# Kernel optimization log

Measured on AMD Instinct MI355X. Metric: run time of the kernel, lower is better.

## Reference

```python
import jax, jax.numpy as jnp
import numpy as np

# ---- constants hard-coded in the torch module ----
NEG_EPS = 1e-30          # eps used in log clamps
TAU = 0.35               # near-field temperature (getattr default)
K0 = 128                 # near-field band width
C_EMBD, N_HEADS, RANK = 768, 12, 32
B, T = 1, 2048


def _lin(k, fin, fout):
    lim = 1.0 / np.sqrt(fin)
    return jax.random.uniform(k, (fin, fout), jnp.float32, -lim, lim)


def _bias(k, fin, fout):
    lim = 1.0 / np.sqrt(fin)
    return jax.random.uniform(k, (fout,), jnp.float32, -lim, lim)


def setup_inputs() -> dict:
    key = jax.random.key(0)
    ks = jax.random.split(key, 24)
    C, H, R = C_EMBD, N_HEADS, RANK
    return {
        "x": jax.random.normal(ks[0], (B, T, C), jnp.float32),
        "Wq_w": _lin(ks[1], C, C), "Wq_b": _bias(ks[2], C, C),
        "Wk_w": _lin(ks[3], C, C), "Wk_b": _bias(ks[4], C, C),
        "Wv_w": _lin(ks[5], C, C), "Wv_b": _bias(ks[6], C, C),
        "Wo_w": _lin(ks[7], C, C), "Wo_b": _bias(ks[8], C, C),
        "Pq_w": _lin(ks[9], C, R),
        "Pk_w": _lin(ks[10], C, R),
        "Pv_w": _lin(ks[11], C, R),
        "up_w": _lin(ks[12], R, C),
        "gate_u": jax.random.normal(ks[13], (H, C // H), jnp.float32),
        "gate_b": jnp.zeros((H,), jnp.float32),
        "Wz_w": _lin(ks[14], 4 * C, C), "Wz_b": _bias(ks[15], 4 * C, C),
    }


def reference(x, Wq_w, Wq_b, Wk_w, Wk_b, Wv_w, Wv_b, Wo_w, Wo_b,
              Pq_w, Pk_w, Pv_w, up_w, gate_u, gate_b, Wz_w, Wz_b):
    Bx, Tx, C = x.shape
    H = gate_u.shape[0]
    D = C // H
    R = Pq_w.shape[1]
    k0 = min(K0, Tx - 1)
    kernel = k0 + 1
    b_scalar = -np.log(max(Tx, 1)).astype(np.float32) if hasattr(np.log(1.0), 'astype') else -np.log(max(Tx, 1))
    b_scalar = jnp.float32(-np.log(max(Tx, 1)))

    # 0) projections + heads
    Q = x @ Wq_w + Wq_b
    K = x @ Wk_w + Wk_b
    V = x @ Wv_w + Wv_b
    heads = lambda z: z.reshape(Bx, Tx, H, D).transpose(0, 2, 1, 3)  # (B,H,T,D)
    Qh, Kh, Vh = heads(Q), heads(K), heads(V)

    idx = jnp.arange(Tx)
    causal = idx[None, :] <= idx[:, None]                  # (T,T)
    band = causal & ((idx[:, None] - idx[None, :]) <= k0)  # banded causal

    # 1) low-rank EA + sigmoid + LASER seed
    Qr, Kr, Vr = Q @ Pq_w, K @ Pk_w, V @ Pv_w              # (B,T,R)
    S = (Qr @ Kr.transpose(0, 2, 1)) * (1.0 / np.sqrt(R))  # (B,T,T)
    # masked logits were -1e9 -> sigmoid == 0 exactly in fp32
    A_seed = jnp.where(causal[None], jax.nn.sigmoid(S * S + b_scalar), 0.0)
    # running causal max over keys, per feature (== amax of causally masked keys)
    m_seed = jax.lax.cummax(Vr, axis=1)                    # (B,T,R)
    Yr = jnp.einsum('bij,bjr->bir', A_seed, jnp.exp(Vr)) * jnp.exp(-m_seed)
    H0 = (jnp.log(jnp.maximum(Yr, NEG_EPS)) + m_seed) @ up_w  # (B,T,C)

    # 2a) near-field banded causal attention (cos^2 / tau, sigmoid, LASER)
    l2n = lambda z: z / jnp.maximum(jnp.linalg.norm(z, axis=-1, keepdims=True), 1e-12)
    cos = jnp.einsum('bhid,bhjd->bhij', l2n(Qh), l2n(Kh))  # (B,H,T,T)
    A_near = jnp.where(band[None, None], jax.nn.sigmoid(cos * cos / TAU + b_scalar), 0.0)
    # sliding-window (width kernel, past-only) max of V per feature
    m_near = jax.lax.reduce_window(
        Vh, -jnp.inf, jax.lax.max,
        window_dimensions=(1, 1, kernel, 1), window_strides=(1, 1, 1, 1),
        padding=[(0, 0), (0, 0), (kernel - 1, 0), (0, 0)])   # (B,H,T,D)
    V_exp = jnp.exp(Vh - m_near)
    Y_near = jnp.einsum('bhij,bhjd->bhid', A_near, V_exp)
    H_near = jnp.log(jnp.maximum(Y_near, NEG_EPS)) + m_near

    # 2b) far-field hierarchical levels: source truncates mid-loop; the
    # accumulator H_far_total_h is initialized to zeros -> contributes zero.
    Ht_h = H_near                                          # (B,H,T,D)

    # 3) head-wise sigmoid gating
    g = jax.nn.sigmoid(jnp.einsum('bhtd,hd->bht', Ht_h, gate_u) + gate_b[None, :, None])
    Ht_h = Ht_h * g[..., None]
    Htilde = Ht_h.transpose(0, 2, 1, 3).reshape(Bx, Tx, C)

    # 4) GRU blend (Wz consumes 4*C features)
    z = jax.nn.sigmoid(jnp.concatenate([x, H0, Htilde, H0 * Htilde], axis=-1) @ Wz_w + Wz_b)
    H_out = (1.0 - z) * H0 + z * Htilde
    return H_out @ Wo_w + Wo_b
```

## Files before the change

### kernel.cpp

```cpp
#include <hip/hip_runtime.h>
#include <math.h>

static constexpr float B_SCALAR    = -7.6246189861593985f;
static constexpr float INV_TAU     = 2.8571428571428571f;
static constexpr float INV_SQRT_R  = 0.17677669529663687f;

typedef __attribute__((ext_vector_type(8))) short bf16x8;
typedef __attribute__((ext_vector_type(4))) float f32x4;

__device__ __forceinline__ unsigned short f2b(float f) {
    union { float f; unsigned int u; } v; v.f = f;
    unsigned int r = v.u + 0x7fffu + ((v.u >> 16) & 1u);
    return (unsigned short)(r >> 16);
}
__device__ __forceinline__ float b2f(unsigned short u) {
    union { unsigned int i; float f; } v; v.i = ((unsigned int)u) << 16; return v.f;
}

typedef const __attribute__((address_space(1))) unsigned int* gp1_t;
typedef __attribute__((address_space(3))) unsigned int* lp3_t;
__device__ __forceinline__ void gload16(const unsigned short* g, unsigned short* l) {
    __builtin_amdgcn_global_load_lds((gp1_t)g, (lp3_t)l, 16, 0, 0);
}

__device__ __forceinline__ bf16x8 frag128(const unsigned short* base, int row, int elem) {
    int byte = (row * 128 + elem * 2) ^ ((row & 7) << 4);
    return *(const bf16x8*)((const char*)base + byte);
}
__device__ __forceinline__ bf16x8 frag384(const unsigned short* base, int row, int elem) {
    int byte = (row * 384 + elem * 2) ^ ((row & 7) << 4);
    return *(const bf16x8*)((const char*)base + byte);
}

template<int MODE, int KZ>
__global__ __launch_bounds__(256) void gemm_mfma(
    const unsigned short* __restrict__ A0, const unsigned short* __restrict__ A1,
    const unsigned short* __restrict__ A2,
    const unsigned short* __restrict__ Bt, const float* __restrict__ bias,
    float* __restrict__ outf, unsigned short* __restrict__ outb,
    float* __restrict__ pbuf, int K, int ldo)
{
    __shared__ unsigned short As[2][64*64];
    __shared__ unsigned short Bs[2][128*64];
    const int tid = threadIdx.x;
    const int lane = tid & 63, wid = tid >> 6;
    const int wr = wid >> 1, wc = wid & 1;
    const int fr = lane & 15, fq = lane >> 4;
    const int lin = blockIdx.y * gridDim.x + blockIdx.x;
    const int chunk = (gridDim.x * gridDim.y) >> 3;
    const int sw = (lin & 7) * chunk + (lin >> 3);
    const int n0 = (sw / gridDim.y) * 128, m0 = (sw % gridDim.y) * 64;
    const int kz = blockIdx.z;
    const int kslice = K / KZ;
    const int kbase = kz * kslice;
    const int nt = kslice / 64;

    f32x4 acc[2][4];
#pragma unroll
    for (int mi = 0; mi < 2; ++mi)
#pragma unroll
        for (int ni = 0; ni < 4; ++ni) acc[mi][ni] = (f32x4){0.f, 0.f, 0.f, 0.f};

    auto stage = [&](int buf, int k0) {
        if (MODE == 1 && k0 >= 2304) {
            int k0l = k0 - 2304;
#pragma unroll
            for (int i = 0; i < 2; ++i) {
                int cb = i * 256 + wid * 64, c = cb + lane;
                int r = c >> 3, col = ((c & 7) ^ (r & 7)) * 8;
                bf16x8 a8 = *(const bf16x8*)&A1[(size_t)(m0 + r) * 768 + k0l + col];
                bf16x8 b8 = *(const bf16x8*)&A2[(size_t)(m0 + r) * 768 + k0l + col];
                bf16x8 p8;
#pragma unroll
                for (int e = 0; e < 8; ++e)
                    p8[e] = (short)f2b(b2f((unsigned short)a8[e]) * b2f((unsigned short)b8[e]));
                *(bf16x8*)&As[buf][(size_t)c * 8] = p8;
            }
        } else {
            const unsigned short* Ap;
            int k0l, ldA;
            if (MODE == 1) {
                int p = k0 / 768;
                Ap = (p == 0) ? A0 : (p == 1) ? A1 : A2;
                k0l = k0 - p * 768; ldA = 768;
            } else { Ap = A0; k0l = k0; ldA = K; }
#pragma unroll
            for (int i = 0; i < 2; ++i) {
                int cb = i * 256 + wid * 64, c = cb + lane;
                int r = c >> 3;
                int col = ((c & 7) ^ (r & 7)) * 8;
                gload16(Ap + (size_t)(m0 + r) * ldA + k0l + col, &As[buf][cb * 8]);
            }
        }
#pragma unroll
        for (int i = 0; i < 4; ++i) {
            int cb = i * 256 + wid * 64, c = cb + lane;
            int r = c >> 3;
            int col = ((c & 7) ^ (r & 7)) * 8;
            gload16(Bt + (size_t)(n0 + r) * K + k0 + col, &Bs[buf][cb * 8]);
        }
    };

    stage(0, kbase);
    asm volatile("s_waitcnt vmcnt(0) lgkmcnt(0)" ::: "memory");
    __builtin_amdgcn_s_barrier();
    __builtin_amdgcn_sched_barrier(0);

    int cur = 0;
    for (int t = 0; t < nt; ++t) {
        if (t + 1 < nt) stage(cur ^ 1, kbase + (t + 1) * 64);
#pragma unroll
        for (int kk = 0; kk < 64; kk += 32) {
            bf16x8 af[2], bfr[4];
#pragma unroll
            for (int mi = 0; mi < 2; ++mi)
                af[mi] = frag128(As[cur], wr*32 + mi*16 + fr, kk + fq*8);
#pragma unroll
            for (int ni = 0; ni < 4; ++ni)
                bfr[ni] = frag128(Bs[cur], wc*64 + ni*16 + fr, kk + fq*8);
#pragma unroll
            for (int mi = 0; mi < 2; ++mi)
#pragma unroll
                for (int ni = 0; ni < 4; ++ni)
                    acc[mi][ni] = __builtin_amdgcn_mfma_f32_16x16x32_bf16(
                        af[mi], bfr[ni], acc[mi][ni], 0, 0, 0);
        }
        asm volatile("s_waitcnt vmcnt(0) lgkmcnt(0)" ::: "memory");
        __builtin_amdgcn_s_barrier();
        __builtin_amdgcn_sched_barrier(0);
        cur ^= 1;
    }
#pragma unroll
    for (int mi = 0; mi < 2; ++mi)
#pragma unroll
        for (int ni = 0; ni < 4; ++ni)
#pragma unroll
            for (int v = 0; v < 4; ++v) {
                int m = m0 + wr*32 + mi*16 + fq*4 + v;
                int n = n0 + wc*64 + ni*16 + fr;
                float val = acc[mi][ni][v];
                if (KZ > 1) {
                    pbuf[((size_t)kz * 2048 + m) * 768 + n] = val;
                } else {
                    float vv = val + bias[n];
                    outf[(size_t)m * ldo + n] = vv;
                    if (MODE == 0) outb[(size_t)m * ldo + n] = f2b(vv);
                }
            }
}

__global__ __launch_bounds__(256) void wz_combine(
    const float* __restrict__ pbuf, const float* __restrict__ bz,
    const float* __restrict__ h0, const float* __restrict__ htl,
    unsigned short* __restrict__ outb)
{
    int i = blockIdx.x * 256 + threadIdx.x;
    if (i >= 2048*768/4) return;
    float4 s = *(const float4*)&pbuf[i*4];
    float4 p1 = *(const float4*)&pbuf[1536*1024 + i*4];
    float4 p2 = *(const float4*)&pbuf[2*1536*1024 + i*4];
    float4 p3 = *(const float4*)&pbuf[3*1536*1024 + i*4];
    s.x += p1.x + p2.x + p3.x; s.y += p1.y + p2.y + p3.y;
    s.z += p1.z + p2.z + p3.z; s.w += p1.w + p2.w + p3.w;
    float4 b = *(const float4*)&bz[(i % 192) * 4];
    float4 a = *(const float4*)&h0[i*4];
    float4 t = *(const float4*)&htl[i*4];
    float z0 = 1.f/(1.f+expf(-(s.x+b.x))), z1 = 1.f/(1.f+expf(-(s.y+b.y)));
    float z2 = 1.f/(1.f+expf(-(s.z+b.z))), z3 = 1.f/(1.f+expf(-(s.w+b.w)));
    outb[i*4+0] = f2b((1.f-z0)*a.x + z0*t.x);
    outb[i*4+1] = f2b((1.f-z1)*a.y + z1*t.y);
    outb[i*4+2] = f2b((1.f-z2)*a.z + z2*t.z);
    outb[i*4+3] = f2b((1.f-z3)*a.w + z3*t.w);
}

__global__ __launch_bounds__(256) void prep_all(
    const float* __restrict__ x, unsigned short* __restrict__ xb,
    const float* __restrict__ wq, const float* __restrict__ wk,
    const float* __restrict__ wv, unsigned short* __restrict__ wqkvT,
    const float* __restrict__ wz, unsigned short* __restrict__ wzT,
    const float* __restrict__ wo, unsigned short* __restrict__ woT,
    const float* __restrict__ pq, const float* __restrict__ pk,
    const float* __restrict__ pv, unsigned short* __restrict__ pT,
    const float* __restrict__ bq, const float* __restrict__ bk,
    const float* __restrict__ bv, float* __restrict__ bqkv)
{
    __shared__ float tile[32][33];
    int b = blockIdx.x;
    if (b < 1536) {
        int i = b * 256 + threadIdx.x;
        float4 v = *(const float4*)&x[i * 4];
        xb[i*4+0] = f2b(v.x); xb[i*4+1] = f2b(v.y);
        xb[i*4+2] = f2b(v.z); xb[i*4+3] = f2b(v.w);
        return;
    }
    b -= 1536;
    const float* src; unsigned short* dst; int K, N, tb;
    if (b < 1728) {
        int sel = b / 576;
        src = (sel == 0) ? wq : (sel == 1) ? wk : wv;
        dst = wqkvT + (size_t)sel * 768 * 768;
        K = 768; N = 768; tb = b - sel * 576;
    } else if (b < 4032) {
        src = wz; dst = wzT; K = 3072; N = 768; tb = b - 1728;
    } else if (b < 4608) {
        src = wo; dst = woT; K = 768; N = 768; tb = b - 4032;
    } else if (b < 4680) {
        int sel = (b - 4608) / 24;
        src = (sel == 0) ? pq : (sel == 1) ? pk : pv;
        dst = pT + (size_t)sel * 32 * 768;
        K = 768; N = 32; tb = (b - 4608) % 24;
    } else {
        int n = (b - 4680) * 256 + threadIdx.x;
        if (n < 2304)
            bqkv[n] = (n < 768) ? bq[n] : (n < 1536) ? bk[n - 768] : bv[n - 1536];
        return;
    }
    int kt = K / 32;
    int kb = (tb % kt) * 32, nb = (tb / kt) * 32;
    int tx = threadIdx.x & 31, ty = threadIdx.x >> 5;
#pragma unroll
    for (int s = 0; s < 32; s += 8)
        tile[ty + s][tx] = src[(size_t)(kb + ty + s) * N + nb + tx];
    __syncthreads();
#pragma unroll
    for (int s = 0; s < 32; s += 8)
        dst[(size_t)(nb + ty + s) * K + kb + tx] = f2b(tile[tx][ty + s]);
}

__device__ void lowrank_body(int b, unsigned char* smem,
    const unsigned short* __restrict__ qkvb, const unsigned short* __restrict__ pT,
    float* __restrict__ pbuf)
{
    unsigned short (*As)[128*64] = (unsigned short(*)[128*64])smem;
    unsigned short (*Bs)[32*64]  = (unsigned short(*)[32*64])(smem + 32768);
    const int tid = threadIdx.x, lane = tid & 63, wid = tid >> 6;
    const int fr = lane & 15, fq = lane >> 4;
    const int m0 = (b & 15) * 128;
    const int sel = (b >> 4) % 3, kz = b / 48;
    const int kbase = kz * 192;

    f32x4 acc[2][2];
#pragma unroll
    for (int mi = 0; mi < 2; ++mi)
#pragma unroll
        for (int ni = 0; ni < 2; ++ni) acc[mi][ni] = (f32x4){0.f,0.f,0.f,0.f};

    auto stage = [&](int buf, int k0) {
#pragma unroll
        for (int i = 0; i < 4; ++i) {
            int cb = i * 256 + wid * 64, c = cb + lane;
            int r = c >> 3, col = ((c & 7) ^ (r & 7)) * 8;
            gload16(qkvb + (size_t)(m0 + r) * 2304 + sel*768 + k0 + col, &As[buf][cb * 8]);
        }
        {
            int cb = wid * 64, c = cb + lane;
            int r = c >> 3, col = ((c & 7) ^ (r & 7)) * 8;
            gload16(pT + (size_t)sel * 32*768 + (size_t)r * 768 + k0 + col, &Bs[buf][cb * 8]);
        }
    };

    stage(0, kbase);
    asm volatile("s_waitcnt vmcnt(0)" ::: "memory");
    __builtin_amdgcn_s_barrier();
    __builtin_amdgcn_sched_barrier(0);

    int cur = 0;
    for (int t = 0; t < 3; ++t) {
        if (t + 1 < 3) stage(cur ^ 1, kbase + (t + 1) * 64);
#pragma unroll
        for (int kk = 0; kk < 64; kk += 32) {
            bf16x8 a[2], bb[2];
#pragma unroll
            for (int mi = 0; mi < 2; ++mi)
                a[mi] = frag128(As[cur], wid*32 + mi*16 + fr, kk + fq*8);
#pragma unroll
            for (int ni = 0; ni < 2; ++ni)
                bb[ni] = frag128(Bs[cur], ni*16 + fr, kk + fq*8);
#pragma unroll
            for (int mi = 0; mi < 2; ++mi)
#pragma unroll
                for (int ni = 0; ni < 2; ++ni)
                    acc[mi][ni] = __builtin_amdgcn_mfma_f32_16x16x32_bf16(
                        a[mi], bb[ni], acc[mi][ni], 0, 0, 0);
        }
        asm volatile("s_waitcnt vmcnt(0)" ::: "memory");
        __builtin_amdgcn_s_barrier();
        __builtin_amdgcn_sched_barrier(0);
        cur ^= 1;
    }
#pragma unroll
    for (int mi = 0; mi < 2; ++mi)
#pragma unroll
        for (int ni = 0; ni < 2; ++ni)
#pragma unroll
            for (int v = 0; v < 4; ++v) {
                int m = m0 + wid*32 + mi*16 + fq*4 + v;
                int n = ni*16 + fr;
                pbuf[((size_t)(kz*3 + sel) * 2048 + m) * 32 + n] = acc[mi][ni][v];
            }
}

__device__ void norms_slide_body(int b, unsigned char* smem,
    const float* __restrict__ qkv,
    unsigned short* __restrict__ qhatb, unsigned short* __restrict__ khatb,
    float* __restrict__ mnear, unsigned short* __restrict__ vexptb)
{
    int tid = threadIdx.x;
    if (b < 6144) {
        int w = b * 4 + (tid >> 6);
        int lane = tid & 63;
        int t = w / 12, h = w - t * 12;
        float q = qkv[t*2304 + h*64 + lane];
        float k = qkv[t*2304 + 768 + h*64 + lane];
        float sq = q*q, sk = k*k;
#pragma unroll
        for (int off = 32; off; off >>= 1) { sq += __shfl_xor(sq, off); sk += __shfl_xor(sk, off); }
        float iq = 1.f / fmaxf(sqrtf(sq), 1e-12f);
        float ik = 1.f / fmaxf(sqrtf(sk), 1e-12f);
        qhatb[(size_t)t*768 + h*64 + lane] = f2b(q * iq);
        khatb[(size_t)t*768 + h*64 + lane] = f2b(k * ik);
        return;
    }
    b -= 6144;
    float (*vs)[64] = (float(*)[64])smem;
    int c0 = (b % 12) * 64, t0 = (b / 12) * 64;
#pragma unroll
    for (int s = 0; s < 12; ++s) {
        int idx = tid + s * 256;
        int rr = idx >> 4, c4 = (idx & 15) * 4;
        int t = t0 - 128 + rr;
        float4 v4;
        if (t < 0) v4 = make_float4(-INFINITY, -INFINITY, -INFINITY, -INFINITY);
        else       v4 = *(const float4*)&qkv[t*2304 + 1536 + c0 + c4];
        *(float4*)&vs[rr][c4] = v4;
    }
    __syncthreads();
    int c = tid & 63, tg = tid >> 6;
    const int TG = tg * 16;
    float core = -INFINITY;
    for (int s = TG + 15; s <= TG + 128; ++s) core = fmaxf(core, vs[s][c]);
    float head[16], tail[16];
    head[15] = -INFINITY;
    float hs = -INFINITY;
#pragma unroll
    for (int u = 14; u >= 0; --u) { hs = fmaxf(hs, vs[TG + u][c]); head[u] = hs; }
    tail[0] = -INFINITY;
    float ts = -INFINITY;
#pragma unroll
    for (int u = 1; u <= 15; ++u) { ts = fmaxf(ts, vs[TG + 128 + u][c]); tail[u] = ts; }
#pragma unroll
    for (int u = 0; u < 16; ++u) {
        int tl = TG + u;
        float m = fmaxf(fmaxf(core, head[u]), tail[u]);
        float v = vs[tl + 128][c];
        int t = t0 + tl;
        mnear[(size_t)t*768 + c0 + c] = m;
        vexptb[(size_t)(c0 + c) * 2048 + t] = f2b(expf(v - m));
    }
}

__global__ __launch_bounds__(256) void lrns_pack(
    const unsigned short* __restrict__ qkvb, const unsigned short* __restrict__ pT,
    float* __restrict__ plr, const float* __restrict__ qkv,
    unsigned short* __restrict__ qhatb, unsigned short* __restrict__ khatb,
    float* __restrict__ mnear, unsigned short* __restrict__ vexptb)
{
    __shared__ unsigned char smem[49152];
    int b = blockIdx.x;
    if (b < 192) lowrank_body(b, smem, qkvb, pT, plr);
    else         norms_slide_body(b - 192, smem, qkv, qhatb, khatb, mnear, vexptb);
}

__global__ __launch_bounds__(256) void lowrank_post(
    const float* __restrict__ pbuf,
    unsigned short* __restrict__ qrb, unsigned short* __restrict__ krb,
    unsigned short* __restrict__ evtb, float* __restrict__ ms)
{
    int b = blockIdx.x, tid = threadIdx.x;
    if (b < 512) {
        int idx = b * 256 + tid;
        int sel = idx >> 16, rem = idx & 65535;
        float s = pbuf[(size_t)(0*3 + sel)*65536 + rem]
                + pbuf[(size_t)(1*3 + sel)*65536 + rem]
                + pbuf[(size_t)(2*3 + sel)*65536 + rem]
                + pbuf[(size_t)(3*3 + sel)*65536 + rem];
        if (sel == 0) qrb[rem] = f2b(s * INV_SQRT_R);
        else          krb[rem] = f2b(s);
        return;
    }
    __shared__ float part[256];
    int r = b - 512;
    int t0 = tid * 8;
    float sv[8], v[8];
    float run = -INFINITY;
#pragma unroll
    for (int e = 0; e < 8; ++e) {
        int t = t0 + e;
        float s = pbuf[(size_t)(0*3 + 2)*65536 + t*32 + r]
                + pbuf[(size_t)(1*3 + 2)*65536 + t*32 + r]
                + pbuf[(size_t)(2*3 + 2)*65536 + t*32 + r]
                + pbuf[(size_t)(3*3 + 2)*65536 + t*32 + r];
        sv[e] = s;
        run = fmaxf(run, s);
        v[e] = run;
    }
    part[tid] = run;
    __syncthreads();
    for (int off = 1; off < 256; off <<= 1) {
        float other = (tid >= off) ? part[tid - off] : -INFINITY;
        __syncthreads();
        part[tid] = fmaxf(part[tid], other);
        __syncthreads();
    }
    float excl = (tid > 0) ? part[tid - 1] : -INFINITY;
#pragma unroll
    for (int e = 0; e < 8; ++e) {
        int t = t0 + e;
        ms[t*32 + r] = fmaxf(v[e], excl);
        evtb[(size_t)r * 2048 + t] = f2b(expf(sv[e]));
    }
}

__device__ void seed_body(int it, int jc, unsigned char* smem,
    const unsigned short* __restrict__ qrb, const unsigned short* __restrict__ krb,
    const unsigned short* __restrict__ evtb, float* __restrict__ partial)
{
    const int i0 = it * 128, j0 = jc * 128;
    unsigned short* Qs = (unsigned short*)smem;
    unsigned short* Ks = (unsigned short*)(smem + 8192);
    unsigned short* Es = (unsigned short*)(smem + 16384);
    unsigned short* Ps = (unsigned short*)(smem + 24576);
    const int tid = threadIdx.x, lane = tid & 63, wid = tid >> 6;
    const int fr = lane & 15, fq = lane >> 4;

#pragma unroll
    for (int s = 0; s < 2; ++s) {
        int cb = s * 256 + wid * 64;
        int c = cb + lane;
        int r = c >> 2, col = (c & 3) * 8;
        gload16(qrb + (size_t)(i0 + r) * 32 + col, &Qs[cb * 8]);
        gload16(krb + (size_t)(j0 + r) * 32 + col, &Ks[cb * 8]);
    }
#pragma unroll
    for (int s = 0; s < 2; ++s) {
        int c = s * 256 + tid;
        int rr = c >> 4, cc = c & 15;
        bf16x8 v = *(const bf16x8*)&evtb[(size_t)rr * 2048 + j0 + cc * 8];
        int byte = (rr * 256 + cc * 16) ^ ((rr & 7) << 4);
        *(bf16x8*)((char*)Es + byte) = v;
    }
    __syncthreads();

    const int wr = wid >> 1, wc = wid & 1;
    bf16x8 af[4], bk[4];
#pragma unroll
    for (int mi = 0; mi < 4; ++mi)
        af[mi] = *(const bf16x8*)&Qs[(wr*64 + mi*16 + fr)*32 + fq*8];
#pragma unroll
    for (int ni = 0; ni < 4; ++ni)
        bk[ni] = *(const bf16x8*)&Ks[(wc*64 + ni*16 + fr)*32 + fq*8];
#pragma unroll
    for (int mi = 0; mi < 4; ++mi)
#pragma unroll
        for (int ni = 0; ni < 4; ++ni) {
            f32x4 s4 = __builtin_amdgcn_mfma_f32_16x16x32_bf16(
                af[mi], bk[ni], (f32x4){0.f,0.f,0.f,0.f}, 0, 0, 0);
#pragma unroll
            for (int v = 0; v < 4; ++v) {
                int row = wr*64 + mi*16 + fq*4 + v;
                int col = wc*64 + ni*16 + fr;
                float a = 0.f;
                if (j0 + col <= i0 + row) {
                    float s = s4[v];
                    a = 1.f / (1.f + expf(-(s*s + B_SCALAR)));
                }
                int byte = (row * 256 + col * 2) ^ ((row & 7) << 4);
                *(unsigned short*)((char*)Ps + byte) = f2b(a);
            }
        }
    __syncthreads();

    f32x4 yacc[2][2];
#pragma unroll
    for (int mi = 0; mi < 2; ++mi)
#pragma unroll
        for (int nf = 0; nf < 2; ++nf) yacc[mi][nf] = (f32x4){0.f,0.f,0.f,0.f};
#pragma unroll
    for (int ks = 0; ks < 4; ++ks) {
        bf16x8 pa[2], eb[2];
#pragma unroll
        for (int mi = 0; mi < 2; ++mi) {
            int row = wid*32 + mi*16 + fr;
            int byte = (row * 256 + ks * 64 + fq * 16) ^ ((row & 7) << 4);
            pa[mi] = *(const bf16x8*)((const char*)Ps + byte);
        }
#pragma unroll
        for (int nf = 0; nf < 2; ++nf) {
            int rrow = nf*16 + fr;
            int byte = (rrow * 256 + ks * 64 + fq * 16) ^ ((rrow & 7) << 4);
            eb[nf] = *(const bf16x8*)((const char*)Es + byte);
        }
#pragma unroll
        for (int mi = 0; mi < 2; ++mi)
#pragma unroll
            for (int nf = 0; nf < 2; ++nf)
                yacc[mi][nf] = __builtin_amdgcn_mfma_f32_16x16x32_bf16(
                    pa[mi], eb[nf], yacc[mi][nf], 0, 0, 0);
    }
    float* pout = partial + ((size_t)(it*16 + jc) * 128) * 32;
#pragma unroll
    for (int mi = 0; mi < 2; ++mi)
#pragma unroll
        for (int nf = 0; nf < 2; ++nf)
#pragma unroll
            for (int v = 0; v < 4; ++v) {
                int row = wid*32 + mi*16 + fq*4 + v;
                int col = nf*16 + fr;
                pout[row*32 + col] = yacc[mi][nf][v];
            }
}

__device__ void near_body(int it, int hh, unsigned char* smem,
    const unsigned short* __restrict__ qhatb, const unsigned short* __restrict__ khatb,
    const unsigned short* __restrict__ vexptb, const float* __restrict__ mnear,
    const float* __restrict__ gu, const float* __restrict__ gb,
    float* __restrict__ hn, unsigned short* __restrict__ htlb)
{
    unsigned short* Qs  = (unsigned short*)smem;
    unsigned short* KPs = (unsigned short*)(smem + 8192);
    unsigned short* Vst = (unsigned short*)(smem + 32768);
    const int i0 = it * 64;
    const int tid = threadIdx.x, lane = tid & 63, wid = tid >> 6;
    const int fr = lane & 15, fq = lane >> 4;

#pragma unroll
    for (int i = 0; i < 2; ++i) {
        int cb = i * 256 + wid * 64, c = cb + lane;
        int r = c >> 3, col = ((c & 7) ^ (r & 7)) * 8;
        gload16(qhatb + (size_t)(i0 + r) * 768 + hh*64 + col, &Qs[cb * 8]);
    }
#pragma unroll
    for (int i = 0; i < 6; ++i) {
        int cb = i * 256 + wid * 64, c = cb + lane;
        int r = c >> 3, col = ((c & 7) ^ (r & 7)) * 8;
        int j = i0 - 128 + r; if (j < 0) j = 0;
        gload16(khatb + (size_t)j * 768 + hh*64 + col, &KPs[cb * 8]);
    }
#pragma unroll
    for (int i = 0; i < 6; ++i) {
        int cb = i * 256 + wid * 64, c = cb + lane;
        int d = c / 24, cc = c - d * 24;
        int ccp = (cc & 24) | ((cc & 7) ^ (d & 7));
        int t = i0 - 128 + ccp * 8; if (t < 0) t = 0;
        gload16(vexptb + (size_t)(hh*64 + d) * 2048 + t, &Vst[cb * 8]);
    }
    __syncthreads();

    f32x4 sacc[4][3];
#pragma unroll
    for (int mi = 0; mi < 4; ++mi)
#pragma unroll
        for (int ni = 0; ni < 3; ++ni) sacc[mi][ni] = (f32x4){0.f,0.f,0.f,0.f};
#pragma unroll
    for (int kt = 0; kt < 2; ++kt) {
        int kk = kt * 32;
        bf16x8 qa[4], kb[3];
#pragma unroll
        for (int mi = 0; mi < 4; ++mi)
            qa[mi] = frag128(Qs, mi*16 + fr, kk + fq*8);
#pragma unroll
        for (int ni = 0; ni < 3; ++ni)
            kb[ni] = frag128(KPs, wid*48 + ni*16 + fr, kk + fq*8);
#pragma unroll
        for (int mi = 0; mi < 4; ++mi)
#pragma unroll
            for (int ni = 0; ni < 3; ++ni)
                sacc[mi][ni] = __builtin_amdgcn_mfma_f32_16x16x32_bf16(
                    qa[mi], kb[ni], sacc[mi][ni], 0, 0, 0);
    }
    __syncthreads();

#pragma unroll
    for (int mi = 0; mi < 4; ++mi)
#pragma unroll
        for (int ni = 0; ni < 3; ++ni)
#pragma unroll
            for (int v = 0; v < 4; ++v) {
                int il = mi*16 + fq*4 + v;
                int jl = wid*48 + ni*16 + fr;
                float s = sacc[mi][ni][v];
                float a = 0.f;
                if (jl >= il && jl <= il + 128 && (i0 - 128 + jl) >= 0)
                    a = 1.f / (1.f + expf(-(s*s*INV_TAU + B_SCALAR)));
                int byte = (il * 384 + jl * 2) ^ ((il & 7) << 4);
                *(unsigned short*)((char*)KPs + byte) = f2b(a);
            }
    __syncthreads();

    f32x4 yacc[4];
#pragma unroll
    for (int nf = 0; nf < 4; ++nf) yacc[nf] = (f32x4){0.f,0.f,0.f,0.f};
#pragma unroll
    for (int ks = 0; ks < 6; ++ks) {
        int kk = ks * 32;
        bf16x8 pa = frag384(KPs, wid*16 + fr, kk + fq*8);
        bf16x8 vb[4];
#pragma unroll
        for (int nf = 0; nf < 4; ++nf)
            vb[nf] = frag384(Vst, nf*16 + fr, kk + fq*8);
#pragma unroll
        for (int nf = 0; nf < 4; ++nf)
            yacc[nf] = __builtin_amdgcn_mfma_f32_16x16x32_bf16(pa, vb[nf], yacc[nf], 0, 0, 0);
    }

    float hv[4][4];
    float sp[4] = {0.f, 0.f, 0.f, 0.f};
#pragma unroll
    for (int nf = 0; nf < 4; ++nf) {
        int d = nf*16 + fr;
        float guv = gu[hh*64 + d];
#pragma unroll
        for (int v = 0; v < 4; ++v) {
            int row = wid*16 + fq*4 + v;
            float y = yacc[nf][v];
            float h = logf(fmaxf(y, 1e-30f)) + mnear[(size_t)(i0 + row)*768 + hh*64 + d];
            hv[nf][v] = h;
            sp[v] = fmaf(h, guv, sp[v]);
        }
    }
#pragma unroll
    for (int off = 1; off < 16; off <<= 1) {
#pragma unroll
        for (int v = 0; v < 4; ++v) sp[v] += __shfl_xor(sp[v], off);
    }
    float gbh = gb[hh];
#pragma unroll
    for (int v = 0; v < 4; ++v) sp[v] = 1.f / (1.f + expf(-(sp[v] + gbh)));
#pragma unroll
    for (int nf = 0; nf < 4; ++nf)
#pragma unroll
        for (int v = 0; v < 4; ++v) {
            int row = wid*16 + fq*4 + v;
            int d = nf*16 + fr;
            size_t idx = (size_t)(i0 + row)*768 + hh*64 + d;
            float htl = hv[nf][v] * sp[v];
            hn[idx] = htl;
            htlb[idx] = f2b(htl);
        }
}

__global__ __launch_bounds__(256) void seednear_pack(
    const unsigned short* __restrict__ qrb, const unsigned short* __restrict__ krb,
    const unsigned short* __restrict__ evtb, float* __restrict__ partial,
    const unsigned short* __restrict__ qhatb, const unsigned short* __restrict__ khatb,
    const unsigned short* __restrict__ vexptb, const float* __restrict__ mnear,
    const float* __restrict__ gu, const float* __restrict__ gb,
    float* __restrict__ hn, unsigned short* __restrict__ htlb)
{
    __shared__ unsigned char smem[57344];
    int b = blockIdx.x;
    if (b < 256) {
        int it = b >> 4, jc = b & 15;
        if (jc > it) return;
        seed_body(it, jc, smem, qrb, krb, evtb, partial);
    } else {
        int idx = b - 256;
        near_body(idx & 31, idx >> 5, smem, qhatb, khatb, vexptb, mnear,
                  gu, gb, hn, htlb);
    }
}

__global__ __launch_bounds__(256) void seed_up(
    const float* __restrict__ partial, const float* __restrict__ ms,
    const float* __restrict__ up, float* __restrict__ h0,
    unsigned short* __restrict__ h0b)
{
    __shared__ float ls[32];
    int t = blockIdx.x, tid = threadIdx.x;
    if (tid < 32) {
        int r = tid;
        int it = t >> 7, row = t & 127;
        float y = 0.f;
        for (int jjc = 0; jjc <= it; ++jjc)
            y += partial[(((size_t)(it*16 + jjc) * 128) + row) * 32 + r];
        float m = ms[t*32 + r];
        ls[r] = logf(fmaxf(y * expf(-m), 1e-30f)) + m;
    }
    __syncthreads();
    for (int c = tid; c < 768; c += 256) {
        float acc = 0.f;
#pragma unroll
        for (int rr = 0; rr < 32; ++rr) acc = fmaf(ls[rr], up[rr*768 + c], acc);
        h0[(size_t)t*768 + c] = acc;
        h0b[(size_t)t*768 + c] = f2b(acc);
    }
}

extern "C" void kernel_launch(void* const* d_in, const int* in_sizes, int n_in,
                              void* d_out, int out_size, void* d_ws, size_t ws_size,
                              hipStream_t stream)
{
    const float* x  = (const float*)d_in[0];
    const float* wq = (const float*)d_in[1];  const float* bq = (const float*)d_in[2];
    const float* wk = (const float*)d_in[3];  const float* bk = (const float*)d_in[4];
    const float* wv = (const float*)d_in[5];  const float* bv = (const float*)d_in[6];
    const float* wo = (const float*)d_in[7];  const float* bo = (const float*)d_in[8];
    const float* pq = (const float*)d_in[9];  const float* pk = (const float*)d_in[10];
    const float* pv = (const float*)d_in[11];
    const float* up = (const float*)d_in[12];
    const float* gu = (const float*)d_in[13]; const float* gb = (const float*)d_in[14];
    const float* wz = (const float*)d_in[15]; const float* bz = (const float*)d_in[16];
    float* out = (float*)d_out;

    float* w = (float*)d_ws;
    float* qkv  = w; w += 2048*2304;
    float* ms   = w; w += 2048*32;
    float* h0   = w; w += 2048*768;
    float* mnear= w; w += 2048*768;
    float* hn   = w; w += 2048*768;
    float* partial = w; w += 16*16*128*32;
    float* pgemm = w; w += 4*2048*768;
    float* plr   = w; w += 4*3*2048*32;
    float* bqkv = w; w += 2304;
    unsigned short* xb     = (unsigned short*)w; w += 2048*768/2;
    unsigned short* qkvb   = (unsigned short*)w; w += 2048*2304/2;
    unsigned short* wqkvT  = (unsigned short*)w; w += 2304*768/2;
    unsigned short* wzT    = (unsigned short*)w; w += 768*3072/2;
    unsigned short* woT    = (unsigned short*)w; w += 768*768/2;
    unsigned short* pT     = (unsigned short*)w; w += 3*32*768/2;
    unsigned short* h0b    = (unsigned short*)w; w += 2048*768/2;
    unsigned short* htlb   = (unsigned short*)w; w += 2048*768/2;
    unsigned short* houtb  = (unsigned short*)w; w += 2048*768/2;
    unsigned short* qrb    = (unsigned short*)w; w += 2048*32/2;
    unsigned short* krb    = (unsigned short*)w; w += 2048*32/2;
    unsigned short* evtb   = (unsigned short*)w; w += 32*2048/2;
    unsigned short* qhatb  = (unsigned short*)w; w += 2048*768/2;
    unsigned short* khatb  = (unsigned short*)w; w += 2048*768/2;
    unsigned short* vexptb = (unsigned short*)w; w += 768*2048/2;

    prep_all<<<6225, 256, 0, stream>>>(x, xb, wq, wk, wv, wqkvT, wz, wzT,
                                       wo, woT, pq, pk, pv, pT, bq, bk, bv, bqkv);

    gemm_mfma<0,1><<<dim3(18,32,1), 256, 0, stream>>>(xb, nullptr, nullptr,
        wqkvT, bqkv, qkv, qkvb, nullptr, 768, 2304);

    lrns_pack<<<6720, 256, 0, stream>>>(qkvb, pT, plr, qkv, qhatb, khatb, mnear, vexptb);

    lowrank_post<<<544, 256, 0, stream>>>(plr, qrb, krb, evtb, ms);

    seednear_pack<<<640, 256, 0, stream>>>(qrb, krb, evtb, partial,
        qhatb, khatb, vexptb, mnear, gu, gb, hn, htlb);

    seed_up<<<2048, 256, 0, stream>>>(partial, ms, up, h0, h0b);

    gemm_mfma<1,4><<<dim3(6,32,4), 256, 0, stream>>>(xb, h0b, htlb,
        wzT, nullptr, nullptr, nullptr, pgemm, 3072, 768);

    wz_combine<<<1536, 256, 0, stream>>>(pgemm, bz, h0, hn, houtb);

    gemm_mfma<2,1><<<dim3(6,32,1), 256, 0, stream>>>(houtb, nullptr, nullptr,
        woT, bo, out, nullptr, nullptr, 768, 768);
}
```

Baseline: 148.9 us.

## Drop fp32 QKV output, read bf16 QKV, split-K the output projection

The QKV GEMM now writes only the bf16 copy, and the norm and sliding-max stages read bf16 instead of the fp32 QKV buffer. This removes a large fp32 store and the matching reloads. The output-projection GEMM is split two ways along K to fill more of the GPU, with a new combine kernel that adds the partials and the bias. For non-Wz modes the wait drops the lgkmcnt, since those modes only use direct global-to-LDS loads. In exchange there is an extra kernel launch, a round trip of partials through memory, and the norms and max now see bf16-rounded values.

Measured after the change: 145.6 us. 2.2% less time.

```diff
diff --git a/kernel.cpp b/kernel.cpp
--- a/kernel.cpp
+++ b/kernel.cpp
@@ -100,9 +100,15 @@
             gload16(Bt + (size_t)(n0 + r) * K + k0 + col, &Bs[buf][cb * 8]);
         }
     };
+    auto wait_all = [&]() {
+        if constexpr (MODE == 1)
+            asm volatile("s_waitcnt vmcnt(0) lgkmcnt(0)" ::: "memory");
+        else
+            asm volatile("s_waitcnt vmcnt(0)" ::: "memory");
+    };
 
     stage(0, kbase);
-    asm volatile("s_waitcnt vmcnt(0) lgkmcnt(0)" ::: "memory");
+    wait_all();
     __builtin_amdgcn_s_barrier();
     __builtin_amdgcn_sched_barrier(0);
 
@@ -125,7 +131,7 @@
                     acc[mi][ni] = __builtin_amdgcn_mfma_f32_16x16x32_bf16(
                         af[mi], bfr[ni], acc[mi][ni], 0, 0, 0);
         }
-        asm volatile("s_waitcnt vmcnt(0) lgkmcnt(0)" ::: "memory");
+        wait_all();
         __builtin_amdgcn_s_barrier();
         __builtin_amdgcn_sched_barrier(0);
         cur ^= 1;
@@ -141,10 +147,10 @@
                 float val = acc[mi][ni][v];
                 if (KZ > 1) {
                     pbuf[((size_t)kz * 2048 + m) * 768 + n] = val;
+                } else if (MODE == 0) {
+                    outb[(size_t)m * ldo + n] = f2b(val + bias[n]);
                 } else {
-                    float vv = val + bias[n];
-                    outf[(size_t)m * ldo + n] = vv;
-                    if (MODE == 0) outb[(size_t)m * ldo + n] = f2b(vv);
+                    outf[(size_t)m * ldo + n] = val + bias[n];
                 }
             }
 }
@@ -171,6 +177,21 @@
     outb[i*4+1] = f2b((1.f-z1)*a.y + z1*t.y);
     outb[i*4+2] = f2b((1.f-z2)*a.z + z2*t.z);
     outb[i*4+3] = f2b((1.f-z3)*a.w + z3*t.w);
+}
+
+__global__ __launch_bounds__(256) void wo_combine(
+    const float* __restrict__ pbuf, const float* __restrict__ bo,
+    float* __restrict__ out)
+{
+    int i = blockIdx.x * 256 + threadIdx.x;
+    if (i >= 2048*768/4) return;
+    float4 s = *(const float4*)&pbuf[i*4];
+    float4 p1 = *(const float4*)&pbuf[1536*1024 + i*4];
+    float4 b = *(const float4*)&bo[(i % 192) * 4];
+    float4 o;
+    o.x = s.x + p1.x + b.x; o.y = s.y + p1.y + b.y;
+    o.z = s.z + p1.z + b.z; o.w = s.w + p1.w + b.w;
+    *(float4*)&out[i*4] = o;
 }
 
 __global__ __launch_bounds__(256) void prep_all(
@@ -301,7 +322,7 @@
 }
 
 __device__ void norms_slide_body(int b, unsigned char* smem,
-    const float* __restrict__ qkv,
+    const unsigned short* __restrict__ qkvb,
     unsigned short* __restrict__ qhatb, unsigned short* __restrict__ khatb,
     float* __restrict__ mnear, unsigned short* __restrict__ vexptb)
 {
@@ -310,8 +331,8 @@
         int w = b * 4 + (tid >> 6);
         int lane = tid & 63;
         int t = w / 12, h = w - t * 12;
-        float q = qkv[t*2304 + h*64 + lane];
-        float k = qkv[t*2304 + 768 + h*64 + lane];
+        float q = b2f(qkvb[(size_t)t*2304 + h*64 + lane]);
+        float k = b2f(qkvb[(size_t)t*2304 + 768 + h*64 + lane]);
         float sq = q*q, sk = k*k;
 #pragma unroll
         for (int off = 32; off; off >>= 1) { sq += __shfl_xor(sq, off); sk += __shfl_xor(sk, off); }
@@ -325,14 +346,18 @@
     float (*vs)[64] = (float(*)[64])smem;
     int c0 = (b % 12) * 64, t0 = (b / 12) * 64;
 #pragma unroll
-    for (int s = 0; s < 12; ++s) {
+    for (int s = 0; s < 6; ++s) {
         int idx = tid + s * 256;
-        int rr = idx >> 4, c4 = (idx & 15) * 4;
+        int rr = idx >> 3, c8 = (idx & 7) * 8;
         int t = t0 - 128 + rr;
-        float4 v4;
-        if (t < 0) v4 = make_float4(-INFINITY, -INFINITY, -INFINITY, -INFINITY);
-        else       v4 = *(const float4*)&qkv[t*2304 + 1536 + c0 + c4];
-        *(float4*)&vs[rr][c4] = v4;
+        if (t < 0) {
+#pragma unroll
+            for (int e = 0; e < 8; ++e) vs[rr][c8 + e] = -INFINITY;
+        } else {
+            bf16x8 v8 = *(const bf16x8*)&qkvb[(size_t)t*2304 + 1536 + c0 + c8];
+#pragma unroll
+            for (int e = 0; e < 8; ++e) vs[rr][c8 + e] = b2f((unsigned short)v8[e]);
+        }
     }
     __syncthreads();
     int c = tid & 63, tg = tid >> 6;
@@ -361,14 +386,14 @@
 
 __global__ __launch_bounds__(256) void lrns_pack(
     const unsigned short* __restrict__ qkvb, const unsigned short* __restrict__ pT,
-    float* __restrict__ plr, const float* __restrict__ qkv,
+    float* __restrict__ plr,
     unsigned short* __restrict__ qhatb, unsigned short* __restrict__ khatb,
     float* __restrict__ mnear, unsigned short* __restrict__ vexptb)
 {
     __shared__ unsigned char smem[49152];
     int b = blockIdx.x;
     if (b < 192) lowrank_body(b, smem, qkvb, pT, plr);
-    else         norms_slide_body(b - 192, smem, qkv, qhatb, khatb, mnear, vexptb);
+    else         norms_slide_body(b - 192, smem, qkvb, qhatb, khatb, mnear, vexptb);
 }
 
 __global__ __launch_bounds__(256) void lowrank_post(
@@ -713,7 +738,6 @@
     float* out = (float*)d_out;
 
     float* w = (float*)d_ws;
-    float* qkv  = w; w += 2048*2304;
     float* ms   = w; w += 2048*32;
     float* h0   = w; w += 2048*768;
     float* mnear= w; w += 2048*768;
@@ -742,9 +766,9 @@
                                        wo, woT, pq, pk, pv, pT, bq, bk, bv, bqkv);
 
     gemm_mfma<0,1><<<dim3(18,32,1), 256, 0, stream>>>(xb, nullptr, nullptr,
-        wqkvT, bqkv, qkv, qkvb, nullptr, 768, 2304);
-
-    lrns_pack<<<6720, 256, 0, stream>>>(qkvb, pT, plr, qkv, qhatb, khatb, mnear, vexptb);
+        wqkvT, bqkv, nullptr, qkvb, nullptr, 768, 2304);
+
+    lrns_pack<<<6720, 256, 0, stream>>>(qkvb, pT, plr, qhatb, khatb, mnear, vexptb);
 
     lowrank_post<<<544, 256, 0, stream>>>(plr, qrb, krb, evtb, ms);
 
@@ -758,6 +782,8 @@
 
     wz_combine<<<1536, 256, 0, stream>>>(pgemm, bz, h0, hn, houtb);
 
-    gemm_mfma<2,1><<<dim3(6,32,1), 256, 0, stream>>>(houtb, nullptr, nullptr,
-        woT, bo, out, nullptr, nullptr, 768, 768);
-}
+    gemm_mfma<2,2><<<dim3(6,32,2), 256, 0, stream>>>(houtb, nullptr, nullptr,
+        woT, nullptr, nullptr, nullptr, pgemm, 768, 768);
+
+    wo_combine<<<1536, 256, 0, stream>>>(pgemm, bo, out);
+}
```
